# Optimization experiments

Measured on AMD Instinct MI355X. Metric: run time of the kernel, lower is better.

## Reference

```python
import jax, jax.numpy as jnp
import numpy as np

FDIM = 512
MAX_LEN = 200
B = 16
K_CELLS = 1024
EPS = 1e-5


def setup_inputs() -> dict:
    key = jax.random.key(0)
    ks = jax.random.split(key, 16)
    s = 0.02
    return {
        "src": jax.random.normal(ks[0], (B, MAX_LEN, 33), jnp.float32),
        "prom": jax.random.normal(ks[1], (B, 32), jnp.float32),
        "atac": jax.random.uniform(ks[2], (B, K_CELLS, MAX_LEN), jnp.float32),
        "mask": jax.random.uniform(ks[3], (B, MAX_LEN), jnp.float32),
        # prom_q: Linear(32, 32*fdim)
        "Wq_p": jax.random.normal(ks[4], (32 * FDIM, 32), jnp.float32) * s,
        "bq_p": jax.random.normal(ks[5], (32 * FDIM,), jnp.float32) * s,
        # enha_q: Linear(33, 32*fdim)
        "Wq_e": jax.random.normal(ks[6], (32 * FDIM, 33), jnp.float32) * s,
        "bq_e": jax.random.normal(ks[7], (32 * FDIM,), jnp.float32) * s,
        # prom_sig: Linear(32, 1)
        "Wsig": jax.random.normal(ks[8], (1, 32), jnp.float32) * s,
        "bsig": jax.random.normal(ks[9], (1,), jnp.float32) * s,
        # encoder: Linear(fdim,128) -> ReLU -> Dropout(eval) -> Linear(128,64)
        "W1": jax.random.normal(ks[10], (128, FDIM), jnp.float32) * s,
        "b1": jax.random.normal(ks[11], (128,), jnp.float32) * s,
        "W2": jax.random.normal(ks[12], (64, 128), jnp.float32) * s,
        "b2": jax.random.normal(ks[13], (64,), jnp.float32) * s,
    }


def reference(src, prom, atac, mask, Wq_p, bq_p, Wq_e, bq_e, Wsig, bsig, W1, b1, W2, b2):
    b = prom.shape[0]
    # prom_qm: [B, fdim, 32]
    prom_qm = (prom @ Wq_p.T + bq_p).reshape(b, FDIM, 32)
    # enha_km: [B, max_len, 32, fdim]
    enha_km = (src @ Wq_e.T + bq_e).reshape(b, MAX_LEN, 32, FDIM)
    # QK = prom_qm[b,f,1,32] @ enha_km.transpose(1,3)[b,f,32,L] -> [B, fdim, L]
    QK = jnp.einsum("bfk,blkf->bfl", prom_qm, enha_km)
    # mask multiply (broadcast over fdim)
    QK = QK * mask[:, None, :]
    # slice off promoter column, LayerNorm over last dim, no affine
    QKs = QK[:, :, 1:MAX_LEN]  # [B, fdim, L-1]
    mu = jnp.mean(QKs, axis=-1, keepdims=True)
    var = jnp.var(QKs, axis=-1, keepdims=True)
    QKs = (QKs - mu) * jax.lax.rsqrt(var + EPS)
    # prom_sig: [B, fdim, 1]
    prom_qms = jnp.einsum("bfk,k->bf", prom_qm, Wsig[0]) + bsig[0]
    # atac: [B, K, L] -> transpose -> [B, L, K]
    atac_t = jnp.swapaxes(atac, 1, 2)
    atac_s = atac_t[:, 1:MAX_LEN, :]  # [B, L-1, K]
    atac_p = atac_t[:, 0, :]          # [B, K]
    # aggregation: [B, fdim, K]
    QKall = jnp.einsum("bfl,blk->bfk", QKs, atac_s) + prom_qms[:, :, None] * atac_p[:, None, :]
    # [B, K, fdim]
    QKall = jnp.swapaxes(QKall, 1, 2)
    # encoder MLP (dropout inactive at eval)
    h = jax.nn.relu(QKall @ W1.T + b1)
    out = h @ W2.T + b2  # [B, K, 64]
    return out
```

## Files before the change

### kernel.cpp

```cpp
#include <hip/hip_runtime.h>

#define B_ 16
#define FDIM_ 512
#define LMAX_ 200
#define KC_ 1024
#define KPAD_ 256

typedef __attribute__((ext_vector_type(8)))  _Float16 f16x8;
typedef __attribute__((ext_vector_type(4)))  float    floatx4;

__device__ __forceinline__ f16x8 ld8f(const float* __restrict__ p) {
    float4 v0 = *(const float4*)p;
    float4 v1 = *(const float4*)(p + 4);
    f16x8 o;
    o[0] = (_Float16)v0.x; o[1] = (_Float16)v0.y;
    o[2] = (_Float16)v0.z; o[3] = (_Float16)v0.w;
    o[4] = (_Float16)v1.x; o[5] = (_Float16)v1.y;
    o[6] = (_Float16)v1.z; o[7] = (_Float16)v1.w;
    return o;
}

__global__ __launch_bounds__(256) void k_prep(
    const float* __restrict__ prom, const float* __restrict__ Wq_p,
    const float* __restrict__ bq_p, const float* __restrict__ Wq_e,
    const float* __restrict__ bq_e, const float* __restrict__ Wsig,
    const float* __restrict__ bsig,
    float* __restrict__ Aout, float* __restrict__ Cout, float* __restrict__ Pout)
{
    int f = blockIdx.x;
    int tid = threadIdx.x;

    __shared__ float Wp[32][33];
    __shared__ float We[32][33];
    __shared__ float promS[16][32];
    __shared__ float pqS[16][33];
    __shared__ float bqpS[32], bqeS[32], wsigS[32];

    for (int i = tid; i < 1024; i += 256)
        Wp[i >> 5][i & 31] = Wq_p[(size_t)f * 1024 + i];
    if (tid < 128) ((float4*)&promS[0][0])[tid] = ((const float4*)prom)[tid];
    for (int i = tid; i < 32 * 33; i += 256) {
        int k = i / 33, j = i - k * 33;
        We[k][j] = Wq_e[((size_t)(k * 512 + f)) * 33 + j];
    }
    if (tid < 32) {
        bqpS[tid]  = bq_p[f * 32 + tid];
        bqeS[tid]  = bq_e[tid * 512 + f];
        wsigS[tid] = Wsig[tid];
    }
    __syncthreads();

    for (int i = tid; i < 512; i += 256) {
        int b = i >> 5, k = i & 31;
        float s = bqpS[k];
        #pragma unroll
        for (int j = 0; j < 32; ++j) s += promS[b][j] * Wp[k][j];
        pqS[b][k] = s;
    }
    __syncthreads();

    for (int i = tid; i < 16 * 33; i += 256) {
        int b = i / 33, j = i - b * 33;
        float s = 0.f;
        #pragma unroll
        for (int k = 0; k < 32; ++k) s += pqS[b][k] * We[k][j];
        Aout[((size_t)(b * 512 + f)) * 33 + j] = s;
    }
    if (tid < 16) {
        int b = tid;
        float c = 0.f, p = bsig[0];
        #pragma unroll
        for (int k = 0; k < 32; ++k) {
            c += pqS[b][k] * bqeS[k];
            p += pqS[b][k] * wsigS[k];
        }
        Cout[b * 512 + f] = c;
        Pout[b * 512 + f] = p;
    }
}

__global__ __launch_bounds__(256) void k_qk_ln(
    const float* __restrict__ src, const float* __restrict__ mask,
    const float* __restrict__ A, const float* __restrict__ C,
    const float* __restrict__ P, _Float16* __restrict__ SB)
{
    __shared__ float srcF[6600];
    __shared__ float maskS[200];

    int tid = threadIdx.x;
    int b = blockIdx.x >> 6;
    int fc = blockIdx.x & 63;
    int f_sub = tid >> 5, l_loc = tid & 31;
    int f = fc * 8 + f_sub;
    int wid = b * 512 + f;

    for (int i = tid; i < 6600; i += 256) srcF[i] = src[(size_t)b * 6600 + i];
    for (int i = tid; i < 200; i += 256)  maskS[i] = mask[b * 200 + i];

    float Ar[33];
    const float* Ap = A + (size_t)wid * 33;
    #pragma unroll
    for (int j = 0; j < 33; ++j) Ar[j] = Ap[j];
    float Cv = C[wid], Pv = P[wid];
    __syncthreads();

    float vals[8];
    float s1 = 0.f, s2 = 0.f;
    #pragma unroll
    for (int t = 0; t < 8; ++t) {
        int l = l_loc + 32 * t;
        float v = 0.f;
        if (l < LMAX_) {
            const float* sp = &srcF[l * 33];
            float s = Cv;
            #pragma unroll
            for (int j = 0; j < 33; ++j) s += sp[j] * Ar[j];
            v = s * maskS[l];
            if (l >= 1) { s1 += v; s2 += v * v; }
        }
        vals[t] = v;
    }
    #pragma unroll
    for (int off = 16; off > 0; off >>= 1) {
        s1 += __shfl_xor(s1, off, 64);
        s2 += __shfl_xor(s2, off, 64);
    }
    float mu  = s1 * (1.f / 199.f);
    float var = s2 * (1.f / 199.f) - mu * mu;
    float inv = 1.0f / sqrtf(var + 1e-5f);

    _Float16* Sp = SB + (size_t)wid * KPAD_;
    #pragma unroll
    for (int t = 0; t < 8; ++t) {
        int l = l_loc + 32 * t;
        float v = (l == 0) ? Pv : ((l < LMAX_) ? (vals[t] - mu) * inv : 0.f);
        Sp[l] = (_Float16)v;
    }
}

__global__ __launch_bounds__(256, 2) void k_fused(
    const float* __restrict__ atac, const _Float16* __restrict__ SB,
    const float* __restrict__ W1, const float* __restrict__ b1,
    const float* __restrict__ W2, const float* __restrict__ b2,
    float* __restrict__ out)
{
    __shared__ _Float16 lds[40960];
    _Float16* Qt = lds;
    _Float16* Ht = lds + 32768;

    int tid = threadIdx.x, lane = tid & 63, wid = tid >> 6;
    int l15 = lane & 15, l4 = lane >> 4;
    int b = blockIdx.x >> 4;
    int row0 = (blockIdx.x & 15) * 64;

    const float*    Ab = atac + ((size_t)b * KC_ + row0) * LMAX_;
    const _Float16* Bb = SB + (size_t)b * FDIM_ * KPAD_;

    floatx4 acc[4][8];
    #pragma unroll
    for (int m = 0; m < 4; ++m)
        #pragma unroll
        for (int n = 0; n < 8; ++n)
            acc[m][n] = (floatx4){0.f, 0.f, 0.f, 0.f};

    #pragma unroll
    for (int ks = 0; ks < 8; ++ks) {
        int kg = ks * 32 + l4 * 8;
        bool inr = kg < LMAX_;
        f16x8 av[4], bv[8];
        #pragma unroll
        for (int m = 0; m < 4; ++m) {
            if (inr) {
                av[m] = ld8f(Ab + (size_t)(m * 16 + l15) * LMAX_ + kg);
            } else {
                #pragma unroll
                for (int j = 0; j < 8; ++j) av[m][j] = (_Float16)0.f;
            }
        }
        #pragma unroll
        for (int n = 0; n < 8; ++n)
            bv[n] = *(const f16x8*)(Bb + (size_t)(wid * 128 + n * 16 + l15) * KPAD_ + kg);
        #pragma unroll
        for (int m = 0; m < 4; ++m)
            #pragma unroll
            for (int n = 0; n < 8; ++n)
                acc[m][n] = __builtin_amdgcn_mfma_f32_16x16x32_f16(
                    av[m], bv[n], acc[m][n], 0, 0, 0);
    }

    #pragma unroll
    for (int m = 0; m < 4; ++m) {
        #pragma unroll
        for (int n = 0; n < 8; ++n) {
            int fcol = wid * 128 + n * 16 + l15;
            int g = fcol >> 3, w = fcol & 7;
            #pragma unroll
            for (int q = 0; q < 4; ++q) {
                int row = m * 16 + l4 * 4 + q;
                Qt[row * 512 + ((g ^ (row & 7)) << 3) + w] = (_Float16)acc[m][n][q];
            }
        }
    }
    __syncthreads();

    floatx4 acc2[4][2];
    #pragma unroll
    for (int m = 0; m < 4; ++m)
        #pragma unroll
        for (int n = 0; n < 2; ++n)
            acc2[m][n] = (floatx4){0.f, 0.f, 0.f, 0.f};

    #pragma unroll
    for (int ks = 0; ks < 16; ++ks) {
        int g = ks * 4 + l4;
        f16x8 av[4], bv[2];
        #pragma unroll
        for (int m = 0; m < 4; ++m) {
            int row = m * 16 + l15;
            av[m] = *(const f16x8*)&Qt[row * 512 + ((g ^ (row & 7)) << 3)];
        }
        #pragma unroll
        for (int n = 0; n < 2; ++n)
            bv[n] = ld8f(W1 + (size_t)(wid * 32 + n * 16 + l15) * 512 + ks * 32 + l4 * 8);
        #pragma unroll
        for (int m = 0; m < 4; ++m)
            #pragma unroll
            for (int n = 0; n < 2; ++n)
                acc2[m][n] = __builtin_amdgcn_mfma_f32_16x16x32_f16(
                    av[m], bv[n], acc2[m][n], 0, 0, 0);
    }

    #pragma unroll
    for (int n = 0; n < 2; ++n) {
        int col = wid * 32 + n * 16 + l15;
        float bb = b1[col];
        int cg = col >> 3, cw = col & 7;
        #pragma unroll
        for (int m = 0; m < 4; ++m) {
            #pragma unroll
            for (int q = 0; q < 4; ++q) {
                int row = m * 16 + l4 * 4 + q;
                float v = fmaxf(acc2[m][n][q] + bb, 0.f);
                Ht[row * 128 + ((cg ^ (row & 7)) << 3) + cw] = (_Float16)v;
            }
        }
    }
    __syncthreads();

    floatx4 acc3[4];
    #pragma unroll
    for (int n = 0; n < 4; ++n) acc3[n] = (floatx4){0.f, 0.f, 0.f, 0.f};
    #pragma unroll
    for (int ks = 0; ks < 4; ++ks) {
        int g = ks * 4 + l4;
        int arow = wid * 16 + l15;
        f16x8 a = *(const f16x8*)&Ht[arow * 128 + ((g ^ (arow & 7)) << 3)];
        #pragma unroll
        for (int n = 0; n < 4; ++n) {
            f16x8 bw = ld8f(W2 + (size_t)(n * 16 + l15) * 128 + ks * 32 + l4 * 8);
            acc3[n] = __builtin_amdgcn_mfma_f32_16x16x32_f16(a, bw, acc3[n], 0, 0, 0);
        }
    }
    #pragma unroll
    for (int n = 0; n < 4; ++n) {
        float bb = b2[n * 16 + l15];
        #pragma unroll
        for (int q = 0; q < 4; ++q) {
            size_t grow = (size_t)b * KC_ + row0 + wid * 16 + l4 * 4 + q;
            out[grow * 64 + n * 16 + l15] = acc3[n][q] + bb;
        }
    }
}

extern "C" void kernel_launch(void* const* d_in, const int* in_sizes, int n_in,
                              void* d_out, int out_size, void* d_ws, size_t ws_size,
                              hipStream_t stream)
{
    const float* src  = (const float*)d_in[0];
    const float* prom = (const float*)d_in[1];
    const float* atac = (const float*)d_in[2];
    const float* mask = (const float*)d_in[3];
    const float* Wq_p = (const float*)d_in[4];
    const float* bq_p = (const float*)d_in[5];
    const float* Wq_e = (const float*)d_in[6];
    const float* bq_e = (const float*)d_in[7];
    const float* Wsig = (const float*)d_in[8];
    const float* bsig = (const float*)d_in[9];
    const float* W1   = (const float*)d_in[10];
    const float* b1   = (const float*)d_in[11];
    const float* W2   = (const float*)d_in[12];
    const float* b2   = (const float*)d_in[13];

    float* ws   = (float*)d_ws;
    float* Abuf = ws;
    float* Cbuf = Abuf + 270336;
    float* Pbuf = Cbuf + 8192;
    _Float16* SB = (_Float16*)(Pbuf + 8192);
    float* outp = (float*)d_out;

    hipLaunchKernelGGL(k_prep, dim3(512), dim3(256), 0, stream,
                       prom, Wq_p, bq_p, Wq_e, bq_e, Wsig, bsig, Abuf, Cbuf, Pbuf);

    hipLaunchKernelGGL(k_qk_ln, dim3(1024), dim3(256), 0, stream,
                       src, mask, Abuf, Cbuf, Pbuf, SB);

    hipLaunchKernelGGL(k_fused, dim3(256), dim3(256), 0, stream,
                       atac, SB, W1, b1, W2, b2, outp);
}
```

Baseline: 58.04 us.

## Fuse prep projection into QK/LayerNorm kernel and trim padded K step

Removes the separate prep kernel and computes each block's projected query, folded enhancer weights, bias term and sigmoid term in shared memory inside the QK/LayerNorm kernel. This drops one launch and the global round trip through the A/C/P workspace buffers. In exchange each of the 16 batch blocks per feature chunk recomputes the Wq_p and Wq_e products, reading the weights redundantly with strided Wq_e loads. Separately, the aggregation GEMM loop runs 7 K-steps instead of 8, skipping the last step that covered only padding beyond length 200.

```diff
diff --git a/kernel.cpp b/kernel.cpp
--- a/kernel.cpp
+++ b/kernel.cpp
@@ -20,89 +20,72 @@
     return o;
 }
 
-__global__ __launch_bounds__(256) void k_prep(
-    const float* __restrict__ prom, const float* __restrict__ Wq_p,
-    const float* __restrict__ bq_p, const float* __restrict__ Wq_e,
-    const float* __restrict__ bq_e, const float* __restrict__ Wsig,
-    const float* __restrict__ bsig,
-    float* __restrict__ Aout, float* __restrict__ Cout, float* __restrict__ Pout)
-{
-    int f = blockIdx.x;
-    int tid = threadIdx.x;
-
-    __shared__ float Wp[32][33];
-    __shared__ float We[32][33];
-    __shared__ float promS[16][32];
-    __shared__ float pqS[16][33];
-    __shared__ float bqpS[32], bqeS[32], wsigS[32];
-
-    for (int i = tid; i < 1024; i += 256)
-        Wp[i >> 5][i & 31] = Wq_p[(size_t)f * 1024 + i];
-    if (tid < 128) ((float4*)&promS[0][0])[tid] = ((const float4*)prom)[tid];
-    for (int i = tid; i < 32 * 33; i += 256) {
-        int k = i / 33, j = i - k * 33;
-        We[k][j] = Wq_e[((size_t)(k * 512 + f)) * 33 + j];
-    }
-    if (tid < 32) {
-        bqpS[tid]  = bq_p[f * 32 + tid];
-        bqeS[tid]  = bq_e[tid * 512 + f];
-        wsigS[tid] = Wsig[tid];
-    }
-    __syncthreads();
-
-    for (int i = tid; i < 512; i += 256) {
-        int b = i >> 5, k = i & 31;
-        float s = bqpS[k];
-        #pragma unroll
-        for (int j = 0; j < 32; ++j) s += promS[b][j] * Wp[k][j];
-        pqS[b][k] = s;
-    }
-    __syncthreads();
-
-    for (int i = tid; i < 16 * 33; i += 256) {
-        int b = i / 33, j = i - b * 33;
-        float s = 0.f;
-        #pragma unroll
-        for (int k = 0; k < 32; ++k) s += pqS[b][k] * We[k][j];
-        Aout[((size_t)(b * 512 + f)) * 33 + j] = s;
-    }
-    if (tid < 16) {
-        int b = tid;
-        float c = 0.f, p = bsig[0];
-        #pragma unroll
-        for (int k = 0; k < 32; ++k) {
-            c += pqS[b][k] * bqeS[k];
-            p += pqS[b][k] * wsigS[k];
-        }
-        Cout[b * 512 + f] = c;
-        Pout[b * 512 + f] = p;
-    }
-}
-
-__global__ __launch_bounds__(256) void k_qk_ln(
-    const float* __restrict__ src, const float* __restrict__ mask,
-    const float* __restrict__ A, const float* __restrict__ C,
-    const float* __restrict__ P, _Float16* __restrict__ SB)
+__global__ __launch_bounds__(256) void k_qk(
+    const float* __restrict__ src, const float* __restrict__ prom,
+    const float* __restrict__ mask,
+    const float* __restrict__ Wq_p, const float* __restrict__ bq_p,
+    const float* __restrict__ Wq_e, const float* __restrict__ bq_e,
+    const float* __restrict__ Wsig, const float* __restrict__ bsig,
+    _Float16* __restrict__ SB)
 {
     __shared__ float srcF[6600];
     __shared__ float maskS[200];
+    __shared__ float promS[32];
+    __shared__ float pqS[8][33];
+    __shared__ float AS[8][34];
+    __shared__ float CS[8], PS[8];
 
     int tid = threadIdx.x;
-    int b = blockIdx.x >> 6;
+    int b  = blockIdx.x >> 6;
     int fc = blockIdx.x & 63;
     int f_sub = tid >> 5, l_loc = tid & 31;
     int f = fc * 8 + f_sub;
-    int wid = b * 512 + f;
 
     for (int i = tid; i < 6600; i += 256) srcF[i] = src[(size_t)b * 6600 + i];
     for (int i = tid; i < 200; i += 256)  maskS[i] = mask[b * 200 + i];
+    if (tid < 32) promS[tid] = prom[b * 32 + tid];
+    __syncthreads();
+
+    {
+        int k = l_loc;
+        const float4* wr4 = (const float4*)(Wq_p + (size_t)(f * 32 + k) * 32);
+        float s = bq_p[f * 32 + k];
+        #pragma unroll
+        for (int j4 = 0; j4 < 8; ++j4) {
+            float4 v = wr4[j4];
+            s += promS[4 * j4 + 0] * v.x + promS[4 * j4 + 1] * v.y
+               + promS[4 * j4 + 2] * v.z + promS[4 * j4 + 3] * v.w;
+        }
+        pqS[f_sub][k] = s;
+    }
+    __syncthreads();
+
+    for (int i = tid; i < 264; i += 256) {
+        int fs = i / 33, j = i - fs * 33;
+        int ff = fc * 8 + fs;
+        float s = 0.f;
+        #pragma unroll
+        for (int k = 0; k < 32; ++k)
+            s += pqS[fs][k] * Wq_e[((size_t)(k * 512 + ff)) * 33 + j];
+        AS[fs][j] = s;
+    }
+    if (tid < 8) {
+        int fs = tid;
+        int ff = fc * 8 + fs;
+        float c = 0.f, p = bsig[0];
+        #pragma unroll
+        for (int k = 0; k < 32; ++k) {
+            c += pqS[fs][k] * bq_e[k * 512 + ff];
+            p += pqS[fs][k] * Wsig[k];
+        }
+        CS[fs] = c; PS[fs] = p;
+    }
+    __syncthreads();
 
     float Ar[33];
-    const float* Ap = A + (size_t)wid * 33;
-    #pragma unroll
-    for (int j = 0; j < 33; ++j) Ar[j] = Ap[j];
-    float Cv = C[wid], Pv = P[wid];
-    __syncthreads();
+    #pragma unroll
+    for (int j = 0; j < 33; ++j) Ar[j] = AS[f_sub][j];
+    float Cv = CS[f_sub], Pv = PS[f_sub];
 
     float vals[8];
     float s1 = 0.f, s2 = 0.f;
@@ -129,7 +112,7 @@
     float var = s2 * (1.f / 199.f) - mu * mu;
     float inv = 1.0f / sqrtf(var + 1e-5f);
 
-    _Float16* Sp = SB + (size_t)wid * KPAD_;
+    _Float16* Sp = SB + ((size_t)(b * 512 + f)) * KPAD_;
     #pragma unroll
     for (int t = 0; t < 8; ++t) {
         int l = l_loc + 32 * t;
@@ -164,7 +147,7 @@
             acc[m][n] = (floatx4){0.f, 0.f, 0.f, 0.f};
 
     #pragma unroll
-    for (int ks = 0; ks < 8; ++ks) {
+    for (int ks = 0; ks < 7; ++ks) {
         int kg = ks * 32 + l4 * 8;
         bool inr = kg < LMAX_;
         f16x8 av[4], bv[8];
@@ -291,18 +274,11 @@
     const float* W2   = (const float*)d_in[12];
     const float* b2   = (const float*)d_in[13];
 
-    float* ws   = (float*)d_ws;
-    float* Abuf = ws;
-    float* Cbuf = Abuf + 270336;
-    float* Pbuf = Cbuf + 8192;
-    _Float16* SB = (_Float16*)(Pbuf + 8192);
+    _Float16* SB = (_Float16*)d_ws;
     float* outp = (float*)d_out;
 
-    hipLaunchKernelGGL(k_prep, dim3(512), dim3(256), 0, stream,
-                       prom, Wq_p, bq_p, Wq_e, bq_e, Wsig, bsig, Abuf, Cbuf, Pbuf);
-
-    hipLaunchKernelGGL(k_qk_ln, dim3(1024), dim3(256), 0, stream,
-                       src, mask, Abuf, Cbuf, Pbuf, SB);
+    hipLaunchKernelGGL(k_qk, dim3(1024), dim3(256), 0, stream,
+                       src, prom, mask, Wq_p, bq_p, Wq_e, bq_e, Wsig, bsig, SB);
 
     hipLaunchKernelGGL(k_fused, dim3(256), dim3(256), 0, stream,
                        atac, SB, W1, b1, W2, b2, outp);
```

Result: faster. 53.62 us (-7.6%).
